# Kernel tuning notes

Measured on AMD Instinct MI355X. Metric: run time of the kernel, lower is better.

The kernel has to match this reference:

```python
import jax, jax.numpy as jnp
import numpy as np

ROUTING_ITERS = 3
SQUASH_EPS = 1e-7


def squash(s):
    # squash along last axis (capsule vector dim); equals squash_axis=-2 in the
    # original [B,1,Nout,D,1] layout since we carry s as [B,Nout,D].
    sq = jnp.sum(s * s, axis=-1, keepdims=True)
    scale = sq / (1.0 + sq) / jnp.sqrt(sq + SQUASH_EPS)
    return scale * s


def setup_inputs() -> dict:
    key = jax.random.key(0)
    k1, k2 = jax.random.split(key)
    B, Nin, Din = 128, 1152, 8
    Nout, D = 10, 16
    x = jax.random.normal(k1, (B, Nin, Din), dtype=jnp.float32)
    # glorot_uniform over fan_in=Din, fan_out=D for the [D,Din] transform
    limit = np.sqrt(6.0 / (Din + D)).astype(np.float32)
    W = jax.random.uniform(k2, (Nin, Nout, D, Din), dtype=jnp.float32,
                           minval=-limit, maxval=limit)
    bias = jnp.zeros((Nout, D), dtype=jnp.float32)
    return {"x": x, "W": W, "bias": bias}


def reference(x, W, bias):
    # u_hat[b,i,j,d] = sum_k W[i,j,d,k] * x[b,i,k]   -> [B, Nin, Nout, D]
    u_hat = jnp.einsum('ijdk,bik->bijd', W, x)
    B, Nin, Nout, D = u_hat.shape
    b = jnp.zeros((B, Nin, Nout), dtype=u_hat.dtype)  # routing logits
    v = None
    for it in range(ROUTING_ITERS):
        c = jax.nn.softmax(b, axis=2)                       # over output capsules
        s = jnp.einsum('bij,bijd->bjd', c, u_hat) + bias    # weighted sum + bias
        v = squash(s)                                       # [B, Nout, D]
        if it < ROUTING_ITERS - 1:
            b = b + jnp.einsum('bijd,bjd->bij', u_hat, v)   # agreement update
    return v
```

## Files before the change

### kernel.cpp

```cpp
#include <hip/hip_runtime.h>

#define B_ 128
#define NIN 1152
#define NOUT 10
#define DDIM 16
#define DK 8
#define TI 9
#define NCH (NIN / TI)
#define PADX 76
#define SLICES 8
#define SCELLS (B_ * NOUT * DDIM)

template<int ITER>
__global__ __launch_bounds__(256, 2)
void caps_pass(const float* __restrict__ x, const float* __restrict__ W,
               const float* __restrict__ vin, float* __restrict__ s_part)
{
    __shared__ float sW[TI * 1280];
    __shared__ float sX[32 * PADX];

    const int ic  = blockIdx.x;
    const int bq  = blockIdx.y;
    const int i0  = ic * TI;
    const int b0  = bq * 32;
    const int tid = threadIdx.x;

    {
        const float4* Wg  = reinterpret_cast<const float4*>(W + (size_t)i0 * 1280);
        float4*       sWf = reinterpret_cast<float4*>(sW);
        for (int t = tid; t < TI * 1280 / 4; t += 256) sWf[t] = Wg[t];
    }
    for (int t = tid; t < 32 * 18; t += 256) {
        int r = t / 18, c4 = t % 18;
        float4 vx = *reinterpret_cast<const float4*>(
            x + (size_t)(b0 + r) * (NIN * DK) + (size_t)i0 * DK + c4 * 4);
        *reinterpret_cast<float4*>(&sX[r * PADX + c4 * 4]) = vx;
    }
    __syncthreads();

    const int bg = tid >> 5;
    const int dg = (tid >> 1) & 15;
    const int jh = tid & 1;

    float vr[4][5];
    if (ITER >= 1) {
#pragma unroll
        for (int bb = 0; bb < 4; ++bb)
#pragma unroll
            for (int jj = 0; jj < 5; ++jj)
                vr[bb][jj] = vin[(size_t)(b0 + bg * 4 + bb) * 160 + (jh * 5 + jj) * 16 + dg];
    }

    float s_acc[4][5];
#pragma unroll
    for (int bb = 0; bb < 4; ++bb)
#pragma unroll
        for (int jj = 0; jj < 5; ++jj) s_acc[bb][jj] = 0.f;

#pragma unroll 1
    for (int il = 0; il < TI; ++il) {
        float xr[4][8];
#pragma unroll
        for (int bb = 0; bb < 4; ++bb) {
            const float4* px = reinterpret_cast<const float4*>(&sX[(bg * 4 + bb) * PADX + il * 8]);
            float4 a = px[0], b = px[1];
            xr[bb][0] = a.x; xr[bb][1] = a.y; xr[bb][2] = a.z; xr[bb][3] = a.w;
            xr[bb][4] = b.x; xr[bb][5] = b.y; xr[bb][6] = b.z; xr[bb][7] = b.w;
        }
        float u[4][5];
#pragma unroll
        for (int jj = 0; jj < 5; ++jj) {
            const int j = jh * 5 + jj;
            const float4* pw = reinterpret_cast<const float4*>(&sW[il * 1280 + j * 128 + dg * 8]);
            float4 w0 = pw[0], w1 = pw[1];
#pragma unroll
            for (int bb = 0; bb < 4; ++bb) {
                float acc = w0.x * xr[bb][0];
                acc = fmaf(w0.y, xr[bb][1], acc);
                acc = fmaf(w0.z, xr[bb][2], acc);
                acc = fmaf(w0.w, xr[bb][3], acc);
                acc = fmaf(w1.x, xr[bb][4], acc);
                acc = fmaf(w1.y, xr[bb][5], acc);
                acc = fmaf(w1.z, xr[bb][6], acc);
                acc = fmaf(w1.w, xr[bb][7], acc);
                u[bb][jj] = acc;
            }
        }

        float c[4][5];
        if (ITER == 0) {
#pragma unroll
            for (int bb = 0; bb < 4; ++bb)
#pragma unroll
                for (int jj = 0; jj < 5; ++jj) c[bb][jj] = 0.1f;
        } else {
            float lp[4][5];
#pragma unroll
            for (int bb = 0; bb < 4; ++bb)
#pragma unroll
                for (int jj = 0; jj < 5; ++jj) lp[bb][jj] = u[bb][jj] * vr[bb][jj];
#pragma unroll
            for (int bb = 0; bb < 4; ++bb)
#pragma unroll
                for (int jj = 0; jj < 5; ++jj) {
                    float t = lp[bb][jj];
                    t += __shfl_xor(t, 2, 64);
                    t += __shfl_xor(t, 4, 64);
                    t += __shfl_xor(t, 8, 64);
                    t += __shfl_xor(t, 16, 64);
                    lp[bb][jj] = t;
                }
#pragma unroll
            for (int bb = 0; bb < 4; ++bb) {
                float mx = fmaxf(fmaxf(fmaxf(lp[bb][0], lp[bb][1]),
                                       fmaxf(lp[bb][2], lp[bb][3])), lp[bb][4]);
                mx = fmaxf(mx, __shfl_xor(mx, 1, 64));
                float e0 = __expf(lp[bb][0] - mx);
                float e1 = __expf(lp[bb][1] - mx);
                float e2 = __expf(lp[bb][2] - mx);
                float e3 = __expf(lp[bb][3] - mx);
                float e4 = __expf(lp[bb][4] - mx);
                float sm = e0 + e1 + e2 + e3 + e4;
                sm += __shfl_xor(sm, 1, 64);
                float inv = 1.0f / sm;
                c[bb][0] = e0 * inv; c[bb][1] = e1 * inv; c[bb][2] = e2 * inv;
                c[bb][3] = e3 * inv; c[bb][4] = e4 * inv;
            }
        }
#pragma unroll
        for (int bb = 0; bb < 4; ++bb)
#pragma unroll
            for (int jj = 0; jj < 5; ++jj)
                s_acc[bb][jj] = fmaf(c[bb][jj], u[bb][jj], s_acc[bb][jj]);
    }

    float* sp = s_part + (size_t)(ic & (SLICES - 1)) * SCELLS;
#pragma unroll
    for (int bb = 0; bb < 4; ++bb)
#pragma unroll
        for (int jj = 0; jj < 5; ++jj)
            atomicAdd(&sp[(b0 + bg * 4 + bb) * 160 + (jh * 5 + jj) * 16 + dg],
                      s_acc[bb][jj]);
}

template<int MODE>
__global__ __launch_bounds__(256)
void caps_squash(float* __restrict__ s_part, const float* __restrict__ bias,
                 const float* __restrict__ v_prev, float* __restrict__ v_out)
{
    const int gid = blockIdx.x * 256 + threadIdx.x;
    const int row = gid >> 4;
    const int d   = gid & 15;
    const int j   = row % NOUT;

    float sd = bias[j * 16 + d];
#pragma unroll
    for (int g = 0; g < SLICES; ++g) sd += s_part[g * SCELLS + gid];
    if (MODE != 2) {
#pragma unroll
        for (int g = 0; g < SLICES; ++g) s_part[g * SCELLS + gid] = 0.f;
    }

    float sq = sd * sd;
    sq += __shfl_xor(sq, 1, 64);
    sq += __shfl_xor(sq, 2, 64);
    sq += __shfl_xor(sq, 4, 64);
    sq += __shfl_xor(sq, 8, 64);

    float scale = sq / ((1.0f + sq) * sqrtf(sq + 1e-7f));
    float v = sd * scale;

    if (MODE == 1) v = v_prev[gid] + v;
    v_out[gid] = v;
}

extern "C" void kernel_launch(void* const* d_in, const int* in_sizes, int n_in,
                              void* d_out, int out_size, void* d_ws, size_t ws_size,
                              hipStream_t stream)
{
    const float* x    = (const float*)d_in[0];
    const float* W    = (const float*)d_in[1];
    const float* bias = (const float*)d_in[2];
    float* out = (float*)d_out;

    float* s_part = (float*)d_ws;
    float* vA     = s_part + SLICES * SCELLS;
    float* vB     = vA + SCELLS;

    hipMemsetAsync(s_part, 0, (size_t)SLICES * SCELLS * sizeof(float), stream);

    dim3 pgrid(NCH, 4);
    caps_pass<0><<<pgrid, 256, 0, stream>>>(x, W, nullptr, s_part);
    caps_squash<0><<<SCELLS / 256, 256, 0, stream>>>(s_part, bias, nullptr, vA);
    caps_pass<1><<<pgrid, 256, 0, stream>>>(x, W, vA, s_part);
    caps_squash<1><<<SCELLS / 256, 256, 0, stream>>>(s_part, bias, vA, vB);
    caps_pass<2><<<pgrid, 256, 0, stream>>>(x, W, vB, s_part);
    caps_squash<2><<<SCELLS / 256, 256, 0, stream>>>(s_part, bias, nullptr, out);
}
```

Baseline: 147.3 us.

## Halve block size, double per-thread d work, use DPP reductions and swizzled LDS

Blocks drop to 128 threads, and each thread now computes two d values per (b, j), which halves the cross-lane reduction depth. Shuffle reductions are replaced with DPP row operations and a ds_swizzle. W is stored in shared memory with an XOR swizzle to avoid bank conflicts. The i-tile shrinks from 9 to 6, giving more blocks (192x4), and the atomic slices grow to 32 to reduce contention, at the cost of a larger memset and a longer squash-side slice sum.

```diff
diff --git a/kernel.cpp b/kernel.cpp
--- a/kernel.cpp
+++ b/kernel.cpp
@@ -1,18 +1,22 @@
 #include <hip/hip_runtime.h>
 
-#define B_ 128
-#define NIN 1152
-#define NOUT 10
-#define DDIM 16
-#define DK 8
-#define TI 9
-#define NCH (NIN / TI)
-#define PADX 76
-#define SLICES 8
-#define SCELLS (B_ * NOUT * DDIM)
+#define TI 6
+#define NCH (1152 / TI)
+#define SLICES 32
+#define SCELLS (128 * 10 * 16)
+#define PADX 52
+
+template<int CTRL>
+__device__ __forceinline__ float dpp_add(float v) {
+    int o = __builtin_amdgcn_update_dpp(0, __float_as_int(v), CTRL, 0xf, 0xf, true);
+    return v + __int_as_float(o);
+}
+__device__ __forceinline__ float swz_xor4(float v) {
+    return __int_as_float(__builtin_amdgcn_ds_swizzle(__float_as_int(v), 0x101F));
+}
 
 template<int ITER>
-__global__ __launch_bounds__(256, 2)
+__global__ __launch_bounds__(128, 2)
 void caps_pass(const float* __restrict__ x, const float* __restrict__ W,
                const float* __restrict__ vin, float* __restrict__ s_part)
 {
@@ -28,62 +32,81 @@
     {
         const float4* Wg  = reinterpret_cast<const float4*>(W + (size_t)i0 * 1280);
         float4*       sWf = reinterpret_cast<float4*>(sW);
-        for (int t = tid; t < TI * 1280 / 4; t += 256) sWf[t] = Wg[t];
-    }
-    for (int t = tid; t < 32 * 18; t += 256) {
-        int r = t / 18, c4 = t % 18;
-        float4 vx = *reinterpret_cast<const float4*>(
-            x + (size_t)(b0 + r) * (NIN * DK) + (size_t)i0 * DK + c4 * 4);
-        *reinterpret_cast<float4*>(&sX[r * PADX + c4 * 4]) = vx;
+        for (int t = tid; t < TI * 320; t += 128) {
+            int il = t / 320, S = t % 320;
+            int Sp = S ^ ((S >> 3) & 1);
+            sWf[il * 320 + Sp] = Wg[t];
+        }
+    }
+    {
+        float4* sXf = reinterpret_cast<float4*>(sX);
+        for (int t = tid; t < 32 * 12; t += 128) {
+            int r = t / 12, c = t % 12;
+            sXf[r * 13 + c] = *reinterpret_cast<const float4*>(
+                x + (size_t)(b0 + r) * 9216 + i0 * 8 + c * 4);
+        }
     }
     __syncthreads();
 
-    const int bg = tid >> 5;
-    const int dg = (tid >> 1) & 15;
-    const int jh = tid & 1;
-
-    float vr[4][5];
+    const int dl = (tid & 3) | ((tid >> 1) & 4);
+    const int jh = (tid >> 2) & 1;
+    const int bL = ((tid >> 4) & 7) * 4;
+
+    float vr[4][5][2];
     if (ITER >= 1) {
 #pragma unroll
         for (int bb = 0; bb < 4; ++bb)
 #pragma unroll
             for (int jj = 0; jj < 5; ++jj)
-                vr[bb][jj] = vin[(size_t)(b0 + bg * 4 + bb) * 160 + (jh * 5 + jj) * 16 + dg];
-    }
-
-    float s_acc[4][5];
+#pragma unroll
+                for (int h = 0; h < 2; ++h)
+                    vr[bb][jj][h] = vin[(size_t)(b0 + bL + bb) * 160 +
+                                        (jh * 5 + jj) * 16 + dl + 8 * h];
+    }
+
+    float s_acc[4][5][2];
 #pragma unroll
     for (int bb = 0; bb < 4; ++bb)
 #pragma unroll
-        for (int jj = 0; jj < 5; ++jj) s_acc[bb][jj] = 0.f;
+        for (int jj = 0; jj < 5; ++jj)
+#pragma unroll
+            for (int h = 0; h < 2; ++h) s_acc[bb][jj][h] = 0.f;
 
 #pragma unroll 1
     for (int il = 0; il < TI; ++il) {
         float xr[4][8];
 #pragma unroll
         for (int bb = 0; bb < 4; ++bb) {
-            const float4* px = reinterpret_cast<const float4*>(&sX[(bg * 4 + bb) * PADX + il * 8]);
+            const float4* px = reinterpret_cast<const float4*>(&sX[(bL + bb) * PADX + il * 8]);
             float4 a = px[0], b = px[1];
             xr[bb][0] = a.x; xr[bb][1] = a.y; xr[bb][2] = a.z; xr[bb][3] = a.w;
             xr[bb][4] = b.x; xr[bb][5] = b.y; xr[bb][6] = b.z; xr[bb][7] = b.w;
         }
-        float u[4][5];
+        float u[4][5][2];
 #pragma unroll
         for (int jj = 0; jj < 5; ++jj) {
-            const int j = jh * 5 + jj;
-            const float4* pw = reinterpret_cast<const float4*>(&sW[il * 1280 + j * 128 + dg * 8]);
-            float4 w0 = pw[0], w1 = pw[1];
-#pragma unroll
-            for (int bb = 0; bb < 4; ++bb) {
-                float acc = w0.x * xr[bb][0];
-                acc = fmaf(w0.y, xr[bb][1], acc);
-                acc = fmaf(w0.z, xr[bb][2], acc);
-                acc = fmaf(w0.w, xr[bb][3], acc);
-                acc = fmaf(w1.x, xr[bb][4], acc);
-                acc = fmaf(w1.y, xr[bb][5], acc);
-                acc = fmaf(w1.z, xr[bb][6], acc);
-                acc = fmaf(w1.w, xr[bb][7], acc);
-                u[bb][jj] = acc;
+#pragma unroll
+            for (int h = 0; h < 2; ++h) {
+                const int j  = jh * 5 + jj;
+                const int d  = dl + 8 * h;
+                const int S0 = j * 32 + d * 2;
+                const int sw = (S0 >> 3) & 1;
+                const float4 w0 = *reinterpret_cast<const float4*>(
+                    &sW[il * 1280 + (S0 ^ sw) * 4]);
+                const float4 w1 = *reinterpret_cast<const float4*>(
+                    &sW[il * 1280 + ((S0 + 1) ^ sw) * 4]);
+#pragma unroll
+                for (int bb = 0; bb < 4; ++bb) {
+                    float acc = w0.x * xr[bb][0];
+                    acc = fmaf(w0.y, xr[bb][1], acc);
+                    acc = fmaf(w0.z, xr[bb][2], acc);
+                    acc = fmaf(w0.w, xr[bb][3], acc);
+                    acc = fmaf(w1.x, xr[bb][4], acc);
+                    acc = fmaf(w1.y, xr[bb][5], acc);
+                    acc = fmaf(w1.z, xr[bb][6], acc);
+                    acc = fmaf(w1.w, xr[bb][7], acc);
+                    u[bb][jj][h] = acc;
+                }
             }
         }
 
@@ -98,30 +121,26 @@
 #pragma unroll
             for (int bb = 0; bb < 4; ++bb)
 #pragma unroll
-                for (int jj = 0; jj < 5; ++jj) lp[bb][jj] = u[bb][jj] * vr[bb][jj];
-#pragma unroll
-            for (int bb = 0; bb < 4; ++bb)
-#pragma unroll
                 for (int jj = 0; jj < 5; ++jj) {
-                    float t = lp[bb][jj];
-                    t += __shfl_xor(t, 2, 64);
-                    t += __shfl_xor(t, 4, 64);
-                    t += __shfl_xor(t, 8, 64);
-                    t += __shfl_xor(t, 16, 64);
+                    float t = fmaf(u[bb][jj][1], vr[bb][jj][1],
+                                   u[bb][jj][0] * vr[bb][jj][0]);
+                    t = dpp_add<0xB1>(t);
+                    t = dpp_add<0x4E>(t);
+                    t = dpp_add<0x128>(t);
                     lp[bb][jj] = t;
                 }
 #pragma unroll
             for (int bb = 0; bb < 4; ++bb) {
                 float mx = fmaxf(fmaxf(fmaxf(lp[bb][0], lp[bb][1]),
                                        fmaxf(lp[bb][2], lp[bb][3])), lp[bb][4]);
-                mx = fmaxf(mx, __shfl_xor(mx, 1, 64));
+                mx = fmaxf(mx, swz_xor4(mx));
                 float e0 = __expf(lp[bb][0] - mx);
                 float e1 = __expf(lp[bb][1] - mx);
                 float e2 = __expf(lp[bb][2] - mx);
                 float e3 = __expf(lp[bb][3] - mx);
                 float e4 = __expf(lp[bb][4] - mx);
                 float sm = e0 + e1 + e2 + e3 + e4;
-                sm += __shfl_xor(sm, 1, 64);
+                sm += swz_xor4(sm);
                 float inv = 1.0f / sm;
                 c[bb][0] = e0 * inv; c[bb][1] = e1 * inv; c[bb][2] = e2 * inv;
                 c[bb][3] = e3 * inv; c[bb][4] = e4 * inv;
@@ -131,7 +150,9 @@
         for (int bb = 0; bb < 4; ++bb)
 #pragma unroll
             for (int jj = 0; jj < 5; ++jj)
-                s_acc[bb][jj] = fmaf(c[bb][jj], u[bb][jj], s_acc[bb][jj]);
+#pragma unroll
+                for (int h = 0; h < 2; ++h)
+                    s_acc[bb][jj][h] = fmaf(c[bb][jj], u[bb][jj][h], s_acc[bb][jj][h]);
     }
 
     float* sp = s_part + (size_t)(ic & (SLICES - 1)) * SCELLS;
@@ -139,8 +160,10 @@
     for (int bb = 0; bb < 4; ++bb)
 #pragma unroll
         for (int jj = 0; jj < 5; ++jj)
-            atomicAdd(&sp[(b0 + bg * 4 + bb) * 160 + (jh * 5 + jj) * 16 + dg],
-                      s_acc[bb][jj]);
+#pragma unroll
+            for (int h = 0; h < 2; ++h)
+                atomicAdd(&sp[(b0 + bL + bb) * 160 + (jh * 5 + jj) * 16 + dl + 8 * h],
+                          s_acc[bb][jj][h]);
 }
 
 template<int MODE>
@@ -150,10 +173,9 @@
 {
     const int gid = blockIdx.x * 256 + threadIdx.x;
     const int row = gid >> 4;
-    const int d   = gid & 15;
-    const int j   = row % NOUT;
-
-    float sd = bias[j * 16 + d];
+    const int j   = row % 10;
+
+    float sd = bias[j * 16 + (gid & 15)];
 #pragma unroll
     for (int g = 0; g < SLICES; ++g) sd += s_part[g * SCELLS + gid];
     if (MODE != 2) {
@@ -190,10 +212,10 @@
     hipMemsetAsync(s_part, 0, (size_t)SLICES * SCELLS * sizeof(float), stream);
 
     dim3 pgrid(NCH, 4);
-    caps_pass<0><<<pgrid, 256, 0, stream>>>(x, W, nullptr, s_part);
+    caps_pass<0><<<pgrid, 128, 0, stream>>>(x, W, nullptr, s_part);
     caps_squash<0><<<SCELLS / 256, 256, 0, stream>>>(s_part, bias, nullptr, vA);
-    caps_pass<1><<<pgrid, 256, 0, stream>>>(x, W, vA, s_part);
+    caps_pass<1><<<pgrid, 128, 0, stream>>>(x, W, vA, s_part);
     caps_squash<1><<<SCELLS / 256, 256, 0, stream>>>(s_part, bias, vA, vB);
-    caps_pass<2><<<pgrid, 256, 0, stream>>>(x, W, vB, s_part);
+    caps_pass<2><<<pgrid, 128, 0, stream>>>(x, W, vB, s_part);
     caps_squash<2><<<SCELLS / 256, 256, 0, stream>>>(s_part, bias, nullptr, out);
 }
```

Result: slower. 181.8 us (+23.4%).
